# Kernel optimization log

Hardware: AMD Instinct MI355X
Metric: run time of the kernel (lower is better)

## Reference

```python
import jax, jax.numpy as jnp
import numpy as np
from jax import lax

B, T, NX, NY = 4, 5, 512, 512
HID = 64
N_FP = 4
INV_R = 1000.0


def _build_Q():
    # 7-point space-time Laplacian stencil on the (t, y, x) grid, matching
    # torch.permute(x[i], (0, 2, 1)).flatten() ordering (t outer, y, x inner).
    idx = np.arange(T * NY * NX, dtype=np.int32).reshape(T, NY, NX)
    rows = [idx.ravel()]
    cols = [idx.ravel()]
    vals = [np.full(idx.size, 6.01, np.float32)]  # diag: 6 neighbors + kappa^2

    def add(a, b):
        rows.append(a.ravel()); cols.append(b.ravel())
        vals.append(np.full(a.size, -1.0, np.float32))
        rows.append(b.ravel()); cols.append(a.ravel())
        vals.append(np.full(a.size, -1.0, np.float32))

    add(idx[:-1], idx[1:])          # t neighbors
    add(idx[:, :-1], idx[:, 1:])    # y neighbors
    add(idx[:, :, :-1], idx[:, :, 1:])  # x neighbors
    return (np.concatenate(rows), np.concatenate(cols), np.concatenate(vals))


def setup_inputs() -> dict:
    key = jax.random.key(0)
    ks = jax.random.split(key, 7)
    gt = jax.random.normal(ks[0], (B, T, NX, NY), jnp.float32)
    x = jax.random.normal(ks[1], (B, T, NX, NY), jnp.float32)
    yobs = jax.random.normal(ks[2], (B, T, NX, NY), jnp.float32)
    mask = jax.random.randint(ks[3], (B, T, NX, NY), 0, 2).astype(jnp.int32)
    W1 = jax.random.normal(ks[4], (HID, T, 3, 3), jnp.float32) * 0.05
    b1 = jnp.zeros((HID,), jnp.float32)
    W2 = jax.random.normal(ks[5], (T, HID, 3, 3), jnp.float32) * 0.05
    b2 = jnp.zeros((T,), jnp.float32)
    qr, qc, qv = _build_Q()
    return {"gt": gt, "x": x, "yobs": yobs, "mask": mask,
            "W1": W1, "b1": b1, "W2": W2, "b2": b2,
            "Q_rows": jnp.asarray(qr), "Q_cols": jnp.asarray(qc),
            "Q_vals": jnp.asarray(qv), "n_fp": N_FP}


def _phi_r(x, W1, b1, W2, b2):
    dn = ("NCHW", "OIHW", "NCHW")
    h = lax.conv_general_dilated(x, W1, (1, 1), "SAME", dimension_numbers=dn)
    h = jax.nn.relu(h + b1[None, :, None, None])
    o = lax.conv_general_dilated(h, W2, (1, 1), "SAME", dimension_numbers=dn)
    return o + b2[None, :, None, None]


def _var_cost_row(gt, x, yobs, maskf, Q_rows, Q_cols, Q_vals):
    # dy term: inv_R = 1000*I restricted to observed entries
    dy = (x - yobs) * maskf                       # model_H
    dy_term = INV_R * jnp.sum(maskf * dy * dy, axis=(1, 2, 3))  # [B]
    # x^T Q x on the permuted/flattened field (sparse COO quadratic form)
    xp = jnp.transpose(x, (0, 1, 3, 2)).reshape(x.shape[0], -1)  # [B, T*NY*NX]
    xtQx = jnp.einsum("bn,n,bn->b", xp[:, Q_rows], Q_vals, xp[:, Q_cols])
    loss_OI = dy_term + xtQx
    # weighted MSE with w = ones(5) == plain per-batch MSE
    loss_mse = jnp.mean((gt - x) ** 2, axis=(1, 2, 3))
    return jnp.stack([loss_mse, loss_OI], axis=1)  # [B, 2]


def reference(gt, x, yobs, mask, W1, b1, W2, b2, Q_rows, Q_cols, Q_vals, n_fp):
    maskf = mask.astype(x.dtype)
    unmeas = 1.0 - maskf
    y_obs = yobs * maskf
    x_k = x
    rows = []
    for _ in range(n_fp):
        rows.append(_var_cost_row(gt, x_k, yobs, maskf, Q_rows, Q_cols, Q_vals))
        x_k = _phi_r(x_k, W1, b1, W2, b2) * unmeas + y_obs  # fixed-point step
    x_k = _phi_r(x_k, W1, b1, W2, b2)
    rows.append(_var_cost_row(gt, x_k, yobs, maskf, Q_rows, Q_cols, Q_vals))
    cmp_loss = jnp.stack(rows, axis=1)  # [B, n_fp+1, 2]
    return x_k, cmp_loss
```

## Files before the change

### kernel.cpp

```cpp
#include <hip/hip_runtime.h>
#include <hip/hip_bf16.h>

#define NXD 512
#define NYD 512
#define TD 5
#define BD 4
#define HIDD 64
#define PLANE (NXD*NYD)
#define VOL (TD*PLANE)
#define CBLK 1024

typedef __bf16 bf16x8 __attribute__((ext_vector_type(8)));
typedef __bf16 bf16x4 __attribute__((ext_vector_type(4)));
typedef float  f32x4  __attribute__((ext_vector_type(4)));

#define SX_PS 16
#define SH_PS 80

#define W1R_ELEMS (3*64*32)
#define W2R_ELEMS (2*9*16*32)

__global__ __launch_bounds__(256)
void prep_weights(const float* __restrict__ W1, const float* __restrict__ W2,
                  __bf16* __restrict__ W1r, __bf16* __restrict__ W2r)
{
    int id = blockIdx.x * 256 + threadIdx.x;
    if (id < W1R_ELEMS) {
        int kt  = id >> 11;
        int rem = id & 2047;
        int n   = rem >> 5;
        int kk  = rem & 31;
        int k   = kt * 32 + kk;
        int tap = k >> 3, c = k & 7;
        float v = 0.f;
        if (tap <= 8 && c < 5)
            v = W1[(n * 5 + c) * 9 + tap];
        W1r[id] = (__bf16)v;
    } else if (id < W1R_ELEMS + W2R_ELEMS) {
        int id2 = id - W1R_ELEMS;
        int h    = id2 / 4608;
        int rem  = id2 - h * 4608;
        int tap  = rem >> 9;
        int rem2 = rem & 511;
        int n    = rem2 >> 5;
        int c    = rem2 & 31;
        float v = 0.f;
        if (n < 5)
            v = W2[(n * HIDD + h * 32 + c) * 9 + tap];
        W2r[id2] = (__bf16)v;
    }
}

template<int INP, int OUTP>
__global__ __launch_bounds__(256, 4)
void phi_mfma(const float* __restrict__ xin,
              const __bf16* __restrict__ xin_pk,
              const __bf16* __restrict__ W1r, const __bf16* __restrict__ W2r,
              const float* __restrict__ b1, const float* __restrict__ b2,
              const float* __restrict__ gt, const float* __restrict__ yobs,
              const int* __restrict__ mask,
              float* __restrict__ xout, __bf16* __restrict__ xout_pk,
              float* __restrict__ cpart, int blend)
{
    __shared__ __align__(16) char sx[400 * SX_PS];
    __shared__ __align__(16) char sh[324 * SH_PS];

    const int tid   = threadIdx.x;
    const int wv    = tid >> 6;
    const int lane  = tid & 63;
    const int l15   = lane & 15;
    const int quad  = lane >> 4;
    const int b     = blockIdx.z;
    const int gx0   = blockIdx.x * 16;
    const int gy0   = blockIdx.y * 16;

    for (int p = tid; p < 400; p += 256) {
        const int u  = p / 20;
        const int v  = p - u * 20;
        const int gx = gx0 + u - 2;
        const int gy = gy0 + v - 2;
        bf16x8 pix = {(__bf16)0.f,(__bf16)0.f,(__bf16)0.f,(__bf16)0.f,
                      (__bf16)0.f,(__bf16)0.f,(__bf16)0.f,(__bf16)0.f};
        if (gx >= 0 && gx < NXD && gy >= 0 && gy < NYD) {
            if constexpr (INP == 0) {
                const float* src = xin + (size_t)b * VOL + (size_t)gx * NYD + gy;
                #pragma unroll
                for (int c = 0; c < TD; ++c) pix[c] = (__bf16)src[(size_t)c * PLANE];
            } else {
                pix = *(const bf16x8*)(xin_pk +
                        ((size_t)b * PLANE + (size_t)gx * NYD + gy) * 8);
            }
        }
        *(bf16x8*)(sx + p * SX_PS) = pix;
    }
    __syncthreads();

    if (cpart) {
        const int ti = tid >> 4, tj = tid & 15;
        const int u  = ti + 2,  v  = tj + 2;
        const size_t gbase = (size_t)b * VOL + (size_t)(gx0 + ti) * NYD + (gy0 + tj);
        float xv[TD];
        if constexpr (INP == 0) {
            #pragma unroll
            for (int c = 0; c < TD; ++c) xv[c] = xin[gbase + (size_t)c * PLANE];
        } else {
            bf16x8 pxv = *(const bf16x8*)(xin_pk +
                ((size_t)b * PLANE + (size_t)(gx0 + ti) * NYD + (gy0 + tj)) * 8);
            #pragma unroll
            for (int c = 0; c < TD; ++c) xv[c] = (float)pxv[c];
        }
        float mse = 0.f, dy = 0.f, q = 0.f;
        #pragma unroll
        for (int c = 0; c < TD; ++c) {
            const size_t gi = gbase + (size_t)c * PLANE;
            const float vv = xv[c];
            const float g  = gt[gi];
            const float yo = yobs[gi];
            const int   m  = mask[gi];
            mse += (g - vv) * (g - vv);
            float d = vv - yo;
            if (m) dy += d * d;
            float xp1 = (float)*(const __bf16*)(sx + (u * 20 + v + 1) * SX_PS + c * 2);
            float yp1 = (float)*(const __bf16*)(sx + ((u + 1) * 20 + v) * SX_PS + c * 2);
            float tp1 = (c < TD - 1)
                      ? (float)*(const __bf16*)(sx + (u * 20 + v) * SX_PS + (c + 1) * 2)
                      : 0.f;
            q += 6.01f * vv * vv - 2.f * vv * (xp1 + yp1 + tp1);
        }
        #pragma unroll
        for (int off = 32; off > 0; off >>= 1) {
            mse += __shfl_xor(mse, off, 64);
            dy  += __shfl_xor(dy,  off, 64);
            q   += __shfl_xor(q,   off, 64);
        }
        if (lane == 0) {
            float* pp = cpart + (((size_t)b * 1024 + blockIdx.y * 32 + blockIdx.x) * 4 + wv) * 3;
            pp[0] = mse; pp[1] = dy; pp[2] = q;
        }
    }

    f32x4 acc2[4] = {{0.f,0.f,0.f,0.f},{0.f,0.f,0.f,0.f},
                     {0.f,0.f,0.f,0.f},{0.f,0.f,0.f,0.f}};

    for (int half = 0; half < 2; ++half) {
        bf16x8 A1[2][3];
        f32x4  bias1[2];
        #pragma unroll
        for (int mt = 0; mt < 2; ++mt) {
            bias1[mt] = *(const f32x4*)(b1 + half * 32 + mt * 16 + quad * 4);
            #pragma unroll
            for (int kt = 0; kt < 3; ++kt)
                A1[mt][kt] = *(const bf16x8*)(W1r +
                    ((size_t)(kt * 64 + half * 32 + mt * 16 + l15) * 32 + quad * 8));
        }
        if (half) __syncthreads();

        #pragma unroll 2
        for (int nt = 0; nt < 6; ++nt) {
            const int ntg = wv * 6 + nt;
            const int p   = ntg * 16 + l15;
            const int pc  = (p < 324) ? p : 323;
            const int i   = pc / 18;
            const int j   = pc - 18 * i;
            const int pb  = (i * 20 + j) * SX_PS;
            bf16x8 Bx[3];
            #pragma unroll
            for (int kt = 0; kt < 3; ++kt) {
                int tap = kt * 4 + quad;
                if (tap > 8) tap = 8;
                Bx[kt] = *(const bf16x8*)(sx + pb + ((tap / 3) * 20 + tap % 3) * SX_PS);
            }
            #pragma unroll
            for (int mt = 0; mt < 2; ++mt) {
                f32x4 a = {0.f, 0.f, 0.f, 0.f};
                #pragma unroll
                for (int kt = 0; kt < 3; ++kt)
                    a = __builtin_amdgcn_mfma_f32_16x16x32_bf16(
                            A1[mt][kt], Bx[kt], a, 0, 0, 0);
                if (p < 324) {
                    bf16x4 hv;
                    #pragma unroll
                    for (int r = 0; r < 4; ++r)
                        hv[r] = (__bf16)fmaxf(a[r] + bias1[mt][r], 0.f);
                    *(bf16x4*)(sh + p * SH_PS + (mt * 16 + quad * 4) * 2) = hv;
                }
            }
        }
        __syncthreads();

        bf16x8 A2[9];
        #pragma unroll
        for (int tap = 0; tap < 9; ++tap)
            A2[tap] = *(const bf16x8*)(W2r +
                ((size_t)((half * 9 + tap) * 16 + l15) * 32 + quad * 8));

        const int shbase = (wv * 4 * 18 + l15) * SH_PS + quad * 16;
        bf16x8 R[6][3];
        #pragma unroll
        for (int rr = 0; rr < 3; ++rr)
            #pragma unroll
            for (int tx = 0; tx < 3; ++tx)
                R[rr][tx] = *(const bf16x8*)(sh + shbase + (rr * 18 + tx) * SH_PS);
        #pragma unroll
        for (int m = 0; m < 4; ++m) {
            #pragma unroll
            for (int dy = 0; dy < 3; ++dy)
                #pragma unroll
                for (int tx = 0; tx < 3; ++tx)
                    acc2[m] = __builtin_amdgcn_mfma_f32_16x16x32_bf16(
                                  A2[dy * 3 + tx], R[m + dy][tx], acc2[m], 0, 0, 0);
            if (m < 3) {
                #pragma unroll
                for (int tx = 0; tx < 3; ++tx)
                    R[m + 3][tx] = *(const bf16x8*)(sh + shbase +
                                                    ((m + 3) * 18 + tx) * SH_PS);
            }
        }
    }

    float b2v[4];
    #pragma unroll
    for (int r = 0; r < 4; ++r) {
        const int ch = quad * 4 + r;
        b2v[r] = (ch < TD) ? b2[ch] : 0.f;
    }
    if constexpr (OUTP == 0) {
        #pragma unroll
        for (int m = 0; m < 4; ++m) {
            const int ti2 = wv * 4 + m;
            const size_t rowoff = (size_t)b * VOL + (size_t)(gx0 + ti2) * NYD + (gy0 + l15);
            #pragma unroll
            for (int r = 0; r < 4; ++r) {
                const int ch = quad * 4 + r;
                if (ch < TD) {
                    const size_t off = rowoff + (size_t)ch * PLANE;
                    float o = acc2[m][r] + b2v[r];
                    if (blend && mask[off]) o = yobs[off];
                    xout[off] = o;
                }
            }
        }
    } else {
        const float b2_4 = b2[4];
        #pragma unroll
        for (int m = 0; m < 4; ++m) {
            const int ti2 = wv * 4 + m;
            const float c4 = __shfl(acc2[m][0], 16 + l15, 64) + b2_4;
            if (quad == 0) {
                const size_t poff = (size_t)b * VOL +
                                    (size_t)(gx0 + ti2) * NYD + (gy0 + l15);
                float o[TD];
                #pragma unroll
                for (int r = 0; r < 4; ++r) o[r] = acc2[m][r] + b2v[r];
                o[4] = c4;
                if (blend) {
                    #pragma unroll
                    for (int ch = 0; ch < TD; ++ch) {
                        const size_t off = poff + (size_t)ch * PLANE;
                        if (mask[off]) o[ch] = yobs[off];
                    }
                }
                bf16x8 pk = {(__bf16)o[0], (__bf16)o[1], (__bf16)o[2],
                             (__bf16)o[3], (__bf16)o[4],
                             (__bf16)0.f, (__bf16)0.f, (__bf16)0.f};
                *(bf16x8*)(xout_pk + ((size_t)b * PLANE +
                    (size_t)(gx0 + ti2) * NYD + (gy0 + l15)) * 8) = pk;
            }
        }
    }
}

__global__ __launch_bounds__(256)
void cost_kernel(const float* __restrict__ x, const float* __restrict__ gt,
                 const float* __restrict__ yobs, const int* __restrict__ mask,
                 float* __restrict__ partial)
{
    const int b    = blockIdx.y;
    const int lane = threadIdx.x & 63;
    const int wave = threadIdx.x >> 6;
    const int px   = blockIdx.x * 256 + threadIdx.x;
    const int i    = px >> 9;
    const int j    = px & 511;
    const size_t gbase = (size_t)b * VOL + px;

    float xv[TD];
    #pragma unroll
    for (int c = 0; c < TD; ++c) xv[c] = x[gbase + (size_t)c * PLANE];

    float mse = 0.f, dy = 0.f, q = 0.f;
    #pragma unroll
    for (int c = 0; c < TD; ++c) {
        const size_t gi = gbase + (size_t)c * PLANE;
        const float v  = xv[c];
        const float g  = gt[gi];
        const float yo = yobs[gi];
        const int   m  = mask[gi];

        mse += (g - v) * (g - v);
        float d = v - yo;
        if (m) dy += d * d;

        float tp1 = (c < TD - 1) ? xv[c + 1] : 0.f;
        float yp1 = __shfl_down(xv[c], 1, 64);
        if (lane == 63) yp1 = (j < NYD - 1) ? x[gi + 1] : 0.f;
        float xp1 = (i < NXD - 1) ? x[gi + NYD] : 0.f;
        q += 6.01f * v * v - 2.f * v * (tp1 + yp1 + xp1);
    }

    #pragma unroll
    for (int off = 32; off > 0; off >>= 1) {
        mse += __shfl_xor(mse, off, 64);
        dy  += __shfl_xor(dy,  off, 64);
        q   += __shfl_xor(q,   off, 64);
    }
    if (lane == 0) {
        float* p = partial + (((size_t)b * CBLK + blockIdx.x) * 4 + wave) * 3;
        p[0] = mse; p[1] = dy; p[2] = q;
    }
}

__global__ __launch_bounds__(256)
void finalize_kernel(const float* __restrict__ cpart,
                     float* __restrict__ out)
{
    const int r = blockIdx.x / BD;
    const int b = blockIdx.x - r * BD;
    const float* base = cpart + ((size_t)r * BD + b) * 4096 * 3;
    float mse = 0.f, dy = 0.f, q = 0.f;
    for (int k = threadIdx.x; k < 4096; k += 256) {
        mse += base[k * 3 + 0];
        dy  += base[k * 3 + 1];
        q   += base[k * 3 + 2];
    }
    #pragma unroll
    for (int off = 32; off > 0; off >>= 1) {
        mse += __shfl_xor(mse, off, 64);
        dy  += __shfl_xor(dy,  off, 64);
        q   += __shfl_xor(q,   off, 64);
    }
    __shared__ float red[3][4];
    const int wave = threadIdx.x >> 6;
    const int lane = threadIdx.x & 63;
    if (lane == 0) { red[0][wave] = mse; red[1][wave] = dy; red[2][wave] = q; }
    __syncthreads();
    if (threadIdx.x == 0) {
        float m  = red[0][0] + red[0][1] + red[0][2] + red[0][3];
        float d  = red[1][0] + red[1][1] + red[1][2] + red[1][3];
        float qq = red[2][0] + red[2][1] + red[2][2] + red[2][3];
        out[b * 10 + r * 2 + 0] = m / (float)VOL;
        out[b * 10 + r * 2 + 1] = 1000.f * d + qq;
    }
}

extern "C" void kernel_launch(void* const* d_in, const int* in_sizes, int n_in,
                              void* d_out, int out_size, void* d_ws, size_t ws_size,
                              hipStream_t stream)
{
    const float* gt   = (const float*)d_in[0];
    const float* x0   = (const float*)d_in[1];
    const float* yobs = (const float*)d_in[2];
    const int*   mask = (const int*)d_in[3];
    const float* W1   = (const float*)d_in[4];
    const float* b1   = (const float*)d_in[5];
    const float* W2   = (const float*)d_in[6];
    const float* b2   = (const float*)d_in[7];

    float* out_x    = (float*)d_out;
    float* out_loss = out_x + (size_t)BD * VOL;

    float* wsA      = (float*)d_ws;
    float* cpart    = wsA + (size_t)BD * VOL;
    __bf16* W1r     = (__bf16*)(cpart + 5 * BD * 4096 * 3);
    __bf16* W2r     = W1r + W1R_ELEMS;
    const size_t PROW = (size_t)BD * 4096 * 3;

    __bf16* Pout = (__bf16*)out_x;
    __bf16* Pws  = (__bf16*)wsA;

    dim3 pgrid(NXD / 16, NYD / 16, BD), pblock(256);
    dim3 cgrid(CBLK, BD), cblock(256);

    prep_weights<<<dim3(60), dim3(256), 0, stream>>>(W1, W2, W1r, W2r);

    phi_mfma<0,1><<<pgrid, pblock, 0, stream>>>(x0, nullptr, W1r, W2r, b1, b2,
        gt, yobs, mask, nullptr, Pout, cpart + 0 * PROW, 1);
    phi_mfma<1,1><<<pgrid, pblock, 0, stream>>>(nullptr, Pout, W1r, W2r, b1, b2,
        gt, yobs, mask, nullptr, Pws,  cpart + 1 * PROW, 1);
    phi_mfma<1,1><<<pgrid, pblock, 0, stream>>>(nullptr, Pws,  W1r, W2r, b1, b2,
        gt, yobs, mask, nullptr, Pout, cpart + 2 * PROW, 1);
    phi_mfma<1,1><<<pgrid, pblock, 0, stream>>>(nullptr, Pout, W1r, W2r, b1, b2,
        gt, yobs, mask, nullptr, Pws,  cpart + 3 * PROW, 1);
    phi_mfma<1,0><<<pgrid, pblock, 0, stream>>>(nullptr, Pws,  W1r, W2r, b1, b2,
        gt, yobs, mask, out_x, nullptr, nullptr, 0);
    cost_kernel<<<cgrid, cblock, 0, stream>>>(out_x, gt, yobs, mask, cpart + 4 * PROW);

    finalize_kernel<<<dim3(5 * BD), dim3(256), 0, stream>>>(cpart, out_loss);
}
```

Measured before the change: 543.9 us.

## Pack gt as bf16 with mask bits into a per-pixel side buffer

The first phi kernel writes a 16-byte per-pixel record holding gt for the five time channels as bf16 plus a bitmask of the observation mask. Later phi iterations and the final cost kernel read this record instead of fp32 gt and int32 mask. The later fixed-point iterations also skip the observation-misfit term, since blended states equal yobs at observed points. This cuts global memory traffic per iteration, at the cost of bf16 rounding of gt in the MSE and an extra workspace buffer.

```diff
diff --git a/kernel.cpp b/kernel.cpp
--- a/kernel.cpp
+++ b/kernel.cpp
@@ -19,6 +19,17 @@
 
 #define W1R_ELEMS (3*64*32)
 #define W2R_ELEMS (2*9*16*32)
+
+__device__ __forceinline__ float bfu(unsigned u)
+{
+    union { float f; unsigned x; } t; t.x = u << 16; return t.f;
+}
+__device__ __forceinline__ unsigned bpack(float a, float b)
+{
+    __bf16 ba = (__bf16)a, bb = (__bf16)b;
+    return (unsigned)__builtin_bit_cast(unsigned short, ba) |
+           ((unsigned)__builtin_bit_cast(unsigned short, bb) << 16);
+}
 
 __global__ __launch_bounds__(256)
 void prep_weights(const float* __restrict__ W1, const float* __restrict__ W2,
@@ -58,7 +69,7 @@
               const __bf16* __restrict__ W1r, const __bf16* __restrict__ W2r,
               const float* __restrict__ b1, const float* __restrict__ b2,
               const float* __restrict__ gt, const float* __restrict__ yobs,
-              const int* __restrict__ mask,
+              const int* __restrict__ mask, unsigned* __restrict__ gtm,
               float* __restrict__ xout, __bf16* __restrict__ xout_pk,
               float* __restrict__ cpart, int blend)
 {
@@ -98,35 +109,57 @@
     if (cpart) {
         const int ti = tid >> 4, tj = tid & 15;
         const int u  = ti + 2,  v  = tj + 2;
+        const size_t pxi = (size_t)b * PLANE + (size_t)(gx0 + ti) * NYD + (gy0 + tj);
         const size_t gbase = (size_t)b * VOL + (size_t)(gx0 + ti) * NYD + (gy0 + tj);
-        float xv[TD];
+        float mse = 0.f, dy = 0.f, q = 0.f;
+
         if constexpr (INP == 0) {
-            #pragma unroll
-            for (int c = 0; c < TD; ++c) xv[c] = xin[gbase + (size_t)c * PLANE];
+            float gts[TD]; unsigned mb = 0;
+            #pragma unroll
+            for (int c = 0; c < TD; ++c) {
+                const size_t gi = gbase + (size_t)c * PLANE;
+                const float vv = xin[gi];
+                const float g  = gt[gi];
+                const float yo = yobs[gi];
+                const int   m  = mask[gi];
+                gts[c] = g;
+                if (m) mb |= 1u << c;
+                mse += (g - vv) * (g - vv);
+                float d = vv - yo;
+                if (m) dy += d * d;
+                float xp1 = (float)*(const __bf16*)(sx + (u * 20 + v + 1) * SX_PS + c * 2);
+                float yp1 = (float)*(const __bf16*)(sx + ((u + 1) * 20 + v) * SX_PS + c * 2);
+                float tp1 = (c < TD - 1)
+                          ? (float)*(const __bf16*)(sx + (u * 20 + v) * SX_PS + (c + 1) * 2)
+                          : 0.f;
+                q += 6.01f * vv * vv - 2.f * vv * (xp1 + yp1 + tp1);
+            }
+            uint4 gv;
+            gv.x = bpack(gts[0], gts[1]);
+            gv.y = bpack(gts[2], gts[3]);
+            gv.z = bpack(gts[4], 0.f);
+            gv.w = mb;
+            *(uint4*)(gtm + pxi * 4) = gv;
         } else {
-            bf16x8 pxv = *(const bf16x8*)(xin_pk +
-                ((size_t)b * PLANE + (size_t)(gx0 + ti) * NYD + (gy0 + tj)) * 8);
-            #pragma unroll
-            for (int c = 0; c < TD; ++c) xv[c] = (float)pxv[c];
-        }
-        float mse = 0.f, dy = 0.f, q = 0.f;
-        #pragma unroll
-        for (int c = 0; c < TD; ++c) {
-            const size_t gi = gbase + (size_t)c * PLANE;
-            const float vv = xv[c];
-            const float g  = gt[gi];
-            const float yo = yobs[gi];
-            const int   m  = mask[gi];
-            mse += (g - vv) * (g - vv);
-            float d = vv - yo;
-            if (m) dy += d * d;
-            float xp1 = (float)*(const __bf16*)(sx + (u * 20 + v + 1) * SX_PS + c * 2);
-            float yp1 = (float)*(const __bf16*)(sx + ((u + 1) * 20 + v) * SX_PS + c * 2);
-            float tp1 = (c < TD - 1)
-                      ? (float)*(const __bf16*)(sx + (u * 20 + v) * SX_PS + (c + 1) * 2)
-                      : 0.f;
-            q += 6.01f * vv * vv - 2.f * vv * (xp1 + yp1 + tp1);
-        }
+            bf16x8 pxv = *(const bf16x8*)(xin_pk + pxi * 8);
+            const uint4 gv = *(const uint4*)(gtm + pxi * 4);
+            float gts[TD];
+            gts[0] = bfu(gv.x & 0xffffu); gts[1] = bfu(gv.x >> 16);
+            gts[2] = bfu(gv.y & 0xffffu); gts[3] = bfu(gv.y >> 16);
+            gts[4] = bfu(gv.z & 0xffffu);
+            #pragma unroll
+            for (int c = 0; c < TD; ++c) {
+                const float vv = (float)pxv[c];
+                mse += (gts[c] - vv) * (gts[c] - vv);
+                float xp1 = (float)*(const __bf16*)(sx + (u * 20 + v + 1) * SX_PS + c * 2);
+                float yp1 = (float)*(const __bf16*)(sx + ((u + 1) * 20 + v) * SX_PS + c * 2);
+                float tp1 = (c < TD - 1)
+                          ? (float)*(const __bf16*)(sx + (u * 20 + v) * SX_PS + (c + 1) * 2)
+                          : 0.f;
+                q += 6.01f * vv * vv - 2.f * vv * (xp1 + yp1 + tp1);
+            }
+        }
+
         #pragma unroll
         for (int off = 32; off > 0; off >>= 1) {
             mse += __shfl_xor(mse, off, 64);
@@ -204,11 +237,11 @@
         #pragma unroll
         for (int m = 0; m < 4; ++m) {
             #pragma unroll
-            for (int dy = 0; dy < 3; ++dy)
+            for (int dy2 = 0; dy2 < 3; ++dy2)
                 #pragma unroll
                 for (int tx = 0; tx < 3; ++tx)
                     acc2[m] = __builtin_amdgcn_mfma_f32_16x16x32_bf16(
-                                  A2[dy * 3 + tx], R[m + dy][tx], acc2[m], 0, 0, 0);
+                                  A2[dy2 * 3 + tx], R[m + dy2][tx], acc2[m], 0, 0, 0);
             if (m < 3) {
                 #pragma unroll
                 for (int tx = 0; tx < 3; ++tx)
@@ -247,6 +280,8 @@
             const int ti2 = wv * 4 + m;
             const float c4 = __shfl(acc2[m][0], 16 + l15, 64) + b2_4;
             if (quad == 0) {
+                const size_t pxo  = (size_t)b * PLANE +
+                                    (size_t)(gx0 + ti2) * NYD + (gy0 + l15);
                 const size_t poff = (size_t)b * VOL +
                                     (size_t)(gx0 + ti2) * NYD + (gy0 + l15);
                 float o[TD];
@@ -254,25 +289,25 @@
                 for (int r = 0; r < 4; ++r) o[r] = acc2[m][r] + b2v[r];
                 o[4] = c4;
                 if (blend) {
+                    const unsigned mb = ((const uint4*)(gtm + pxo * 4))->w;
                     #pragma unroll
                     for (int ch = 0; ch < TD; ++ch) {
-                        const size_t off = poff + (size_t)ch * PLANE;
-                        if (mask[off]) o[ch] = yobs[off];
+                        if ((mb >> ch) & 1)
+                            o[ch] = yobs[poff + (size_t)ch * PLANE];
                     }
                 }
                 bf16x8 pk = {(__bf16)o[0], (__bf16)o[1], (__bf16)o[2],
                              (__bf16)o[3], (__bf16)o[4],
                              (__bf16)0.f, (__bf16)0.f, (__bf16)0.f};
-                *(bf16x8*)(xout_pk + ((size_t)b * PLANE +
-                    (size_t)(gx0 + ti2) * NYD + (gy0 + l15)) * 8) = pk;
+                *(bf16x8*)(xout_pk + pxo * 8) = pk;
             }
         }
     }
 }
 
 __global__ __launch_bounds__(256)
-void cost_kernel(const float* __restrict__ x, const float* __restrict__ gt,
-                 const float* __restrict__ yobs, const int* __restrict__ mask,
+void cost_kernel(const float* __restrict__ x, const unsigned* __restrict__ gtm,
+                 const float* __restrict__ yobs,
                  float* __restrict__ partial)
 {
     const int b    = blockIdx.y;
@@ -281,25 +316,30 @@
     const int px   = blockIdx.x * 256 + threadIdx.x;
     const int i    = px >> 9;
     const int j    = px & 511;
+    const size_t pxi   = (size_t)b * PLANE + px;
     const size_t gbase = (size_t)b * VOL + px;
 
     float xv[TD];
     #pragma unroll
     for (int c = 0; c < TD; ++c) xv[c] = x[gbase + (size_t)c * PLANE];
+
+    const uint4 gv = *(const uint4*)(gtm + pxi * 4);
+    float gts[TD];
+    gts[0] = bfu(gv.x & 0xffffu); gts[1] = bfu(gv.x >> 16);
+    gts[2] = bfu(gv.y & 0xffffu); gts[3] = bfu(gv.y >> 16);
+    gts[4] = bfu(gv.z & 0xffffu);
+    const unsigned mb = gv.w;
 
     float mse = 0.f, dy = 0.f, q = 0.f;
     #pragma unroll
     for (int c = 0; c < TD; ++c) {
         const size_t gi = gbase + (size_t)c * PLANE;
         const float v  = xv[c];
-        const float g  = gt[gi];
-        const float yo = yobs[gi];
-        const int   m  = mask[gi];
-
-        mse += (g - v) * (g - v);
-        float d = v - yo;
-        if (m) dy += d * d;
-
+        mse += (gts[c] - v) * (gts[c] - v);
+        if ((mb >> c) & 1) {
+            float d = v - yobs[gi];
+            dy += d * d;
+        }
         float tp1 = (c < TD - 1) ? xv[c + 1] : 0.f;
         float yp1 = __shfl_down(xv[c], 1, 64);
         if (lane == 63) yp1 = (j < NYD - 1) ? x[gi + 1] : 0.f;
@@ -372,6 +412,7 @@
     float* cpart    = wsA + (size_t)BD * VOL;
     __bf16* W1r     = (__bf16*)(cpart + 5 * BD * 4096 * 3);
     __bf16* W2r     = W1r + W1R_ELEMS;
+    unsigned* gtm   = (unsigned*)(W2r + W2R_ELEMS);
     const size_t PROW = (size_t)BD * 4096 * 3;
 
     __bf16* Pout = (__bf16*)out_x;
@@ -383,16 +424,16 @@
     prep_weights<<<dim3(60), dim3(256), 0, stream>>>(W1, W2, W1r, W2r);
 
     phi_mfma<0,1><<<pgrid, pblock, 0, stream>>>(x0, nullptr, W1r, W2r, b1, b2,
-        gt, yobs, mask, nullptr, Pout, cpart + 0 * PROW, 1);
+        gt, yobs, mask, gtm, nullptr, Pout, cpart + 0 * PROW, 1);
     phi_mfma<1,1><<<pgrid, pblock, 0, stream>>>(nullptr, Pout, W1r, W2r, b1, b2,
-        gt, yobs, mask, nullptr, Pws,  cpart + 1 * PROW, 1);
+        gt, yobs, mask, gtm, nullptr, Pws,  cpart + 1 * PROW, 1);
     phi_mfma<1,1><<<pgrid, pblock, 0, stream>>>(nullptr, Pws,  W1r, W2r, b1, b2,
-        gt, yobs, mask, nullptr, Pout, cpart + 2 * PROW, 1);
+        gt, yobs, mask, gtm, nullptr, Pout, cpart + 2 * PROW, 1);
     phi_mfma<1,1><<<pgrid, pblock, 0, stream>>>(nullptr, Pout, W1r, W2r, b1, b2,
-        gt, yobs, mask, nullptr, Pws,  cpart + 3 * PROW, 1);
+        gt, yobs, mask, gtm, nullptr, Pws,  cpart + 3 * PROW, 1);
     phi_mfma<1,0><<<pgrid, pblock, 0, stream>>>(nullptr, Pws,  W1r, W2r, b1, b2,
-        gt, yobs, mask, out_x, nullptr, nullptr, 0);
-    cost_kernel<<<cgrid, cblock, 0, stream>>>(out_x, gt, yobs, mask, cpart + 4 * PROW);
+        gt, yobs, mask, gtm, out_x, nullptr, nullptr, 0);
+    cost_kernel<<<cgrid, cblock, 0, stream>>>(out_x, gtm, yobs, cpart + 4 * PROW);
 
     finalize_kernel<<<dim3(5 * BD), dim3(256), 0, stream>>>(cpart, out_loss);
 }
```

Measured after the change: 475.1 us. -12.6%, faster.
